# Kernel tuning notes

Hardware: AMD Instinct MI355X
Metric: run time of the kernel (lower is better)

Reference implementation:

```python
import jax, jax.numpy as jnp
import numpy as np

B, S, D = 4, 2048, 1024
H = 16
HD = D // H

def setup_inputs() -> dict:
    key = jax.random.key(0)
    ks = jax.random.split(key, 6)
    s = 0.02
    return {
        "input_tensor": jax.random.normal(ks[0], (B, S, D), dtype=jnp.float32),
        "Wq": jax.random.normal(ks[1], (D, D), dtype=jnp.float32) * s,
        "Wk": jax.random.normal(ks[2], (D, D), dtype=jnp.float32) * s,
        "Wv": jax.random.normal(ks[3], (D, D), dtype=jnp.float32) * s,
        "Wo": jax.random.normal(ks[4], (D, D), dtype=jnp.float32) * s,
        "bo": jax.random.normal(ks[5], (D,), dtype=jnp.float32) * s,
    }

def reference(input_tensor, Wq, Wk, Wv, Wo, bo):
    b, n, _ = input_tensor.shape
    # projections (nn.Linear: x @ W.T; bias=False for qkv)
    q = jnp.einsum('bnd,ed->bne', input_tensor, Wq).reshape(b, n, H, HD).transpose(0, 2, 1, 3)
    k = jnp.einsum('bnd,ed->bne', input_tensor, Wk).reshape(b, n, H, HD).transpose(0, 2, 1, 3)
    v = jnp.einsum('bnd,ed->bne', input_tensor, Wv).reshape(b, n, H, HD).transpose(0, 2, 1, 3)
    scores = jnp.einsum('bhqd,bhkd->bhqk', q, k)  # [B,H,S,S]
    causal = jnp.triu(jnp.ones((n, n), dtype=bool), k=1)
    scores = jnp.where(causal, -jnp.inf, scores)
    weights = jax.nn.softmax(scores / jnp.sqrt(jnp.float32(HD)), axis=-1)
    ctx = jnp.einsum('bhqk,bhkd->bhqd', weights, v)  # [B,H,S,HD]
    ctx = ctx.transpose(0, 2, 1, 3).reshape(b, n, D)
    return jnp.einsum('bnd,ed->bne', ctx, Wo) + bo
```

## Files before the change

kernel.cpp:

```cpp
#include <hip/hip_runtime.h>
#include <stdint.h>

#define S_LEN 2048
#define DIM   1024
#define NH    16
#define HD    64
#define BATCH 4
#define M_ROWS (BATCH * S_LEN)
#define PSTR  136

typedef __attribute__((ext_vector_type(8))) __bf16 bf16x8;
typedef __attribute__((ext_vector_type(4))) float  f32x4;

union Frag { bf16x8 v; uint4 q; };

__device__ __forceinline__ ushort f2bf(float f) {
  union { float f; unsigned u; } x; x.f = f;
  unsigned r = x.u + 0x7fffu + ((x.u >> 16) & 1u);
  return (ushort)(r >> 16);
}
__device__ __forceinline__ ushort f2bf_n(float f) {
  union { __bf16 b; ushort u; } x; x.b = (__bf16)f; return x.u;
}

__device__ __forceinline__ f32x4 mfma16(const Frag& a, const Frag& b, f32x4 c) {
  return __builtin_amdgcn_mfma_f32_16x16x32_bf16(a.v, b.v, c, 0, 0, 0);
}

__device__ __forceinline__ void gld_lds16(const ushort* g, ushort* l) {
  __builtin_amdgcn_global_load_lds(
      (__attribute__((address_space(1))) void*)g,
      (__attribute__((address_space(3))) void*)l, 16, 0, 0);
}

__global__ void cast_x_kernel(const float* __restrict__ src, ushort* __restrict__ dst) {
  int i = blockIdx.x * 256 + threadIdx.x;
  float4 f = ((const float4*)src)[i];
  ushort4 u; u.x = f2bf(f.x); u.y = f2bf(f.y); u.z = f2bf(f.z); u.w = f2bf(f.w);
  ((ushort4*)dst)[i] = u;
}

__global__ void cast_w_kernel(const float* __restrict__ w0, const float* __restrict__ w1,
                              const float* __restrict__ w2, const float* __restrict__ w3,
                              ushort* __restrict__ d0, ushort* __restrict__ d1,
                              ushort* __restrict__ d2, ushort* __restrict__ d3) {
  const float* s; ushort* d;
  int z = blockIdx.y;
  if (z == 0) { s = w0; d = d0; } else if (z == 1) { s = w1; d = d1; }
  else if (z == 2) { s = w2; d = d2; } else { s = w3; d = d3; }
  int i = blockIdx.x * 256 + threadIdx.x;
  float4 f = ((const float4*)s)[i];
  ushort4 u; u.x = f2bf(f.x); u.y = f2bf(f.y); u.z = f2bf(f.z); u.w = f2bf(f.w);
  ((ushort4*)d)[i] = u;
}

template <int MODE>
__global__ __launch_bounds__(256)
void gemm_bk64(const ushort* __restrict__ A,
               const ushort* __restrict__ B0, const ushort* __restrict__ B1,
               const ushort* __restrict__ B2,
               ushort* __restrict__ Qb, ushort* __restrict__ Kb, ushort* __restrict__ Vtb,
               float* __restrict__ outf, const float* __restrict__ bias, float scaleq) {
  __shared__ __align__(16) ushort As[128 * 64];
  __shared__ __align__(16) ushort Bs[128 * 64];
  const int K = DIM;
  int lane = threadIdx.x & 63, wave = threadIdx.x >> 6;
  int quad = lane >> 4, l15 = lane & 15;
  int rowBase = blockIdx.y * 128;
  int wsel, colBase;
  const ushort* Bt;
  if (MODE == 0) {
    wsel = blockIdx.x >> 3;
    colBase = (blockIdx.x & 7) * 128;
    Bt = (wsel == 0) ? B0 : (wsel == 1) ? B1 : B2;
  } else {
    wsel = 0;
    colBase = blockIdx.x * 128;
    Bt = B0;
  }
  int wm = (wave >> 1) * 64, wn = (wave & 1) * 64;

  const ushort* Ag = A + (size_t)rowBase * K;
  const ushort* Bg = Bt + (size_t)colBase * K;

  f32x4 acc[4][4];
#pragma unroll
  for (int i = 0; i < 4; i++)
#pragma unroll
    for (int j = 0; j < 4; j++) acc[i][j] = (f32x4){0.f, 0.f, 0.f, 0.f};

  for (int k0 = 0; k0 < K; k0 += 64) {
#pragma unroll
    for (int cc = 0; cc < 4; ++cc) {
      int c = wave * 4 + cc;
      int s = c * 64 + lane;
      int row = s >> 3;
      int c8 = (s & 7) ^ (row & 7);
      gld_lds16(Ag + (size_t)row * K + k0 + c8 * 8, &As[c * 512]);
      gld_lds16(Bg + (size_t)row * K + k0 + c8 * 8, &Bs[c * 512]);
    }
    __syncthreads();
    Frag af[4][2], bf[4][2];
#pragma unroll
    for (int t = 0; t < 4; t++) {
      int ar = wm + t * 16 + l15;
      int br = wn + t * 16 + l15;
#pragma unroll
      for (int kk = 0; kk < 2; kk++) {
        af[t][kk].q = *(const uint4*)&As[ar * 64 + (((kk * 4 + quad) ^ (ar & 7))) * 8];
        bf[t][kk].q = *(const uint4*)&Bs[br * 64 + (((kk * 4 + quad) ^ (br & 7))) * 8];
      }
    }
#pragma unroll
    for (int kk = 0; kk < 2; kk++)
#pragma unroll
      for (int i = 0; i < 4; i++)
#pragma unroll
        for (int j = 0; j < 4; j++) acc[i][j] = mfma16(af[i][kk], bf[j][kk], acc[i][j]);
    __syncthreads();
  }

#pragma unroll
  for (int i = 0; i < 4; i++) {
    int rowt = wm + i * 16 + quad * 4;
#pragma unroll
    for (int j = 0; j < 4; j++) {
      int e = colBase + wn + j * 16 + l15;
      if (MODE == 0) {
        int h = e >> 6, hd = e & 63;
        if (wsel < 2) {
          ushort* dst = wsel ? Kb : Qb;
          float sc = wsel ? 1.f : scaleq;
#pragma unroll
          for (int r = 0; r < 4; r++) {
            int m = rowBase + rowt + r;
            int b = m >> 11, s = m & (S_LEN - 1);
            dst[((size_t)((b * NH + h) * S_LEN + s) << 6) + hd] = f2bf(acc[i][j][r] * sc);
          }
        } else {
          int m0 = rowBase + rowt;
          int b = m0 >> 11, s0 = m0 & (S_LEN - 1);
          ushort4 u;
          u.x = f2bf(acc[i][j][0]); u.y = f2bf(acc[i][j][1]);
          u.z = f2bf(acc[i][j][2]); u.w = f2bf(acc[i][j][3]);
          *(ushort4*)&Vtb[((size_t)((b * NH + h) * HD + hd) << 11) + s0] = u;
        }
      } else {
        float bv = bias[e];
#pragma unroll
        for (int r = 0; r < 4; r++) {
          int m = rowBase + rowt + r;
          outf[(size_t)m * DIM + e] = acc[i][j][r] + bv;
        }
      }
    }
  }
}

__global__ __launch_bounds__(256)
void flash_attn(const ushort* __restrict__ Qb, const ushort* __restrict__ Kb,
                const ushort* __restrict__ Vtb, ushort* __restrict__ Ctx) {
  __shared__ __align__(16) ushort Ks[128 * 64];
  __shared__ __align__(16) ushort Vs[64 * 128];
  __shared__ __align__(16) ushort Ps[4][16 * PSTR];

  int lane = threadIdx.x & 63, wave = threadIdx.x >> 6;
  int quad = lane >> 4, l15 = lane & 15;
  int bh = blockIdx.x;
  int qt = (gridDim.y - 1) - blockIdx.y;
  int q0 = qt * 128, wq0 = wave * 32;

  const ushort* Qh = Qb + (size_t)bh * S_LEN * HD;
  const ushort* Kh = Kb + (size_t)bh * S_LEN * HD;
  const ushort* Vh = Vtb + (size_t)bh * HD * S_LEN;

#pragma unroll
  for (int cc = 0; cc < 4; ++cc) {
    int c = wave * 4 + cc;
    int s = c * 64 + lane;
    int row = s >> 3;
    int c8 = (s & 7) ^ (row & 7);
    gld_lds16(Qh + (size_t)(q0 + row) * HD + c8 * 8, &Ks[c * 512]);
  }
  __syncthreads();
  Frag qf[2][2];
#pragma unroll
  for (int it = 0; it < 2; ++it)
#pragma unroll
    for (int ks = 0; ks < 2; ++ks) {
      int row = wq0 + it * 16 + l15;
      int c8 = (ks * 4 + quad) ^ (row & 7);
      qf[it][ks].q = *(const uint4*)&Ks[row * 64 + c8 * 8];
    }
  __syncthreads();

  float lst[2] = {0.f, 0.f};
  f32x4 oacc[2][4];
#pragma unroll
  for (int it = 0; it < 2; ++it)
#pragma unroll
    for (int dt = 0; dt < 4; ++dt) oacc[it][dt] = (f32x4){0.f, 0.f, 0.f, 0.f};

  ushort* Pw = Ps[wave];

  for (int kt = 0; kt <= qt; ++kt) {
#pragma unroll
    for (int cc = 0; cc < 4; ++cc) {
      int c = wave * 4 + cc;
      int s = c * 64 + lane;
      int krow = s >> 3;
      int kc8 = (s & 7) ^ (krow & 7);
      gld_lds16(Kh + (size_t)(kt * 128 + krow) * HD + kc8 * 8, &Ks[c * 512]);
      int vrow = s >> 4;
      int vc8 = (s & 15) ^ (vrow & 15);
      gld_lds16(Vh + (size_t)vrow * S_LEN + kt * 128 + vc8 * 8, &Vs[c * 512]);
    }
    __syncthreads();

    f32x4 sacc[2][8];
#pragma unroll
    for (int jt = 0; jt < 8; ++jt) {
      int row = jt * 16 + l15;
      Frag kf0, kf1;
      kf0.q = *(const uint4*)&Ks[row * 64 + ((quad) ^ (row & 7)) * 8];
      kf1.q = *(const uint4*)&Ks[row * 64 + ((4 + quad) ^ (row & 7)) * 8];
#pragma unroll
      for (int it = 0; it < 2; ++it) {
        f32x4 a = (f32x4){0.f, 0.f, 0.f, 0.f};
        a = mfma16(kf0, qf[it][0], a);
        a = mfma16(kf1, qf[it][1], a);
        sacc[it][jt] = a;
      }
    }

    if (kt == qt) {
#pragma unroll
      for (int it = 0; it < 2; ++it)
#pragma unroll
        for (int jt = 0; jt < 8; ++jt)
#pragma unroll
          for (int r = 0; r < 4; ++r)
            if (jt * 16 + quad * 4 + r > wq0 + it * 16 + l15)
              sacc[it][jt][r] = -1e30f;
    }

#pragma unroll
    for (int it = 0; it < 2; ++it) {
      float ps = 0.f;
#pragma unroll
      for (int jt = 0; jt < 8; ++jt) {
        float p0 = exp2f(sacc[it][jt][0]);
        float p1 = exp2f(sacc[it][jt][1]);
        float p2 = exp2f(sacc[it][jt][2]);
        float p3 = exp2f(sacc[it][jt][3]);
        ps += (p0 + p1) + (p2 + p3);
        ushort4 u; u.x = f2bf_n(p0); u.y = f2bf_n(p1); u.z = f2bf_n(p2); u.w = f2bf_n(p3);
        *(ushort4*)&Pw[l15 * PSTR + jt * 16 + quad * 4] = u;
      }
      ps += __shfl_xor(ps, 16);
      ps += __shfl_xor(ps, 32);
      lst[it] += ps;

      Frag pf[4];
#pragma unroll
      for (int ks = 0; ks < 4; ++ks)
        pf[ks].q = *(const uint4*)&Pw[l15 * PSTR + ks * 32 + quad * 8];

#pragma unroll
      for (int dt = 0; dt < 4; ++dt) {
        f32x4 a = oacc[it][dt];
#pragma unroll
        for (int ks = 0; ks < 4; ++ks) {
          int row = dt * 16 + l15;
          Frag vf;
          vf.q = *(const uint4*)&Vs[row * 128 + (((ks * 4 + quad) ^ (row & 15))) * 8];
          a = mfma16(pf[ks], vf, a);
        }
        oacc[it][dt] = a;
      }
    }
    __syncthreads();
  }

  int b = bh >> 4, h = bh & 15;
#pragma unroll
  for (int it = 0; it < 2; ++it) {
    float linv = 1.f / lst[it];
    float lr[4];
#pragma unroll
    for (int r = 0; r < 4; ++r) lr[r] = __shfl(linv, quad * 4 + r);
#pragma unroll
    for (int r = 0; r < 4; ++r) {
      int qg = q0 + wq0 + it * 16 + quad * 4 + r;
      size_t base = ((size_t)(b * S_LEN + qg)) * DIM + h * HD;
#pragma unroll
      for (int dt = 0; dt < 4; ++dt)
        Ctx[base + dt * 16 + l15] = f2bf_n(oacc[it][dt][r] * lr[r]);
    }
  }
}

extern "C" void kernel_launch(void* const* d_in, const int* in_sizes, int n_in,
                              void* d_out, int out_size, void* d_ws, size_t ws_size,
                              hipStream_t stream) {
  (void)in_sizes; (void)n_in; (void)out_size; (void)ws_size;
  const float* x  = (const float*)d_in[0];
  const float* Wq = (const float*)d_in[1];
  const float* Wk = (const float*)d_in[2];
  const float* Wv = (const float*)d_in[3];
  const float* Wo = (const float*)d_in[4];
  const float* bo = (const float*)d_in[5];
  float* out = (float*)d_out;

  ushort* Xb  = (ushort*)d_ws;
  ushort* Wqb = Xb  + (size_t)M_ROWS * DIM;
  ushort* Wkb = Wqb + (size_t)DIM * DIM;
  ushort* Wvb = Wkb + (size_t)DIM * DIM;
  ushort* Wob = Wvb + (size_t)DIM * DIM;
  ushort* Qb  = Wob + (size_t)DIM * DIM;
  ushort* Kb  = Qb  + (size_t)M_ROWS * DIM;
  ushort* Vtb = Kb  + (size_t)M_ROWS * DIM;
  ushort* Ctx = Vtb + (size_t)M_ROWS * DIM;

  const float SCALE_Q = 0.18033688011112042f;

  cast_x_kernel<<<dim3(M_ROWS * DIM / 1024), 256, 0, stream>>>(x, Xb);
  cast_w_kernel<<<dim3(DIM * DIM / 1024, 4), 256, 0, stream>>>(Wq, Wk, Wv, Wo, Wqb, Wkb, Wvb, Wob);

  gemm_bk64<0><<<dim3(24, 64), 256, 0, stream>>>(Xb, Wqb, Wkb, Wvb, Qb, Kb, Vtb,
                                                 nullptr, nullptr, SCALE_Q);

  flash_attn<<<dim3(BATCH * NH, S_LEN / 128), 256, 0, stream>>>(Qb, Kb, Vtb, Ctx);

  gemm_bk64<1><<<dim3(8, 64), 256, 0, stream>>>(Ctx, Wob, nullptr, nullptr, nullptr, nullptr,
                                                nullptr, out, bo, 1.0f);
}
```

Before: 265.7 us.

## Reuse K smem for P, store Q/K row-major, remap GEMM blocks per XCD

The QKV GEMM now writes Q and K in plain [B*S, D] row-major layout instead of head-major, which makes those epilogue stores contiguous, and flash attention reads them with a DIM stride. The per-wave P staging buffer is removed and P is written into the K shared-memory tile after an extra barrier, with an XOR swizzle replacing the padded stride. This cuts LDS use so more blocks fit per CU, and the launch bound requests 4. GEMM block indices are also remapped so blocks dispatched to the same XCD share row tiles for L2 reuse. The cost is one more __syncthreads per KV tile in attention.

```diff
diff --git a/kernel.cpp b/kernel.cpp
--- a/kernel.cpp
+++ b/kernel.cpp
@@ -7,7 +7,6 @@
 #define HD    64
 #define BATCH 4
 #define M_ROWS (BATCH * S_LEN)
-#define PSTR  136
 
 typedef __attribute__((ext_vector_type(8))) __bf16 bf16x8;
 typedef __attribute__((ext_vector_type(4))) float  f32x4;
@@ -66,16 +65,23 @@
   const int K = DIM;
   int lane = threadIdx.x & 63, wave = threadIdx.x >> 6;
   int quad = lane >> 4, l15 = lane & 15;
-  int rowBase = blockIdx.y * 128;
+
+  const int GX = (MODE == 0) ? 24 : 8;
+  int lin = blockIdx.x + GX * blockIdx.y;
+  int xcd = lin & 7, idx = lin >> 3;
+  int by = xcd * 8 + idx / GX;
+  int bx = idx % GX;
+
+  int rowBase = by * 128;
   int wsel, colBase;
   const ushort* Bt;
   if (MODE == 0) {
-    wsel = blockIdx.x >> 3;
-    colBase = (blockIdx.x & 7) * 128;
+    wsel = bx >> 3;
+    colBase = (bx & 7) * 128;
     Bt = (wsel == 0) ? B0 : (wsel == 1) ? B1 : B2;
   } else {
     wsel = 0;
-    colBase = blockIdx.x * 128;
+    colBase = bx * 128;
     Bt = B0;
   }
   int wm = (wave >> 1) * 64, wn = (wave & 1) * 64;
@@ -127,17 +133,16 @@
     for (int j = 0; j < 4; j++) {
       int e = colBase + wn + j * 16 + l15;
       if (MODE == 0) {
-        int h = e >> 6, hd = e & 63;
         if (wsel < 2) {
           ushort* dst = wsel ? Kb : Qb;
           float sc = wsel ? 1.f : scaleq;
 #pragma unroll
           for (int r = 0; r < 4; r++) {
-            int m = rowBase + rowt + r;
-            int b = m >> 11, s = m & (S_LEN - 1);
-            dst[((size_t)((b * NH + h) * S_LEN + s) << 6) + hd] = f2bf(acc[i][j][r] * sc);
+            size_t m = (size_t)(rowBase + rowt + r);
+            dst[m * DIM + e] = f2bf(acc[i][j][r] * sc);
           }
         } else {
+          int h = e >> 6, hd = e & 63;
           int m0 = rowBase + rowt;
           int b = m0 >> 11, s0 = m0 & (S_LEN - 1);
           ushort4 u;
@@ -157,21 +162,21 @@
   }
 }
 
-__global__ __launch_bounds__(256)
+__global__ __launch_bounds__(256, 4)
 void flash_attn(const ushort* __restrict__ Qb, const ushort* __restrict__ Kb,
                 const ushort* __restrict__ Vtb, ushort* __restrict__ Ctx) {
   __shared__ __align__(16) ushort Ks[128 * 64];
   __shared__ __align__(16) ushort Vs[64 * 128];
-  __shared__ __align__(16) ushort Ps[4][16 * PSTR];
 
   int lane = threadIdx.x & 63, wave = threadIdx.x >> 6;
   int quad = lane >> 4, l15 = lane & 15;
   int bh = blockIdx.x;
   int qt = (gridDim.y - 1) - blockIdx.y;
   int q0 = qt * 128, wq0 = wave * 32;
-
-  const ushort* Qh = Qb + (size_t)bh * S_LEN * HD;
-  const ushort* Kh = Kb + (size_t)bh * S_LEN * HD;
+  int b = bh >> 4, h = bh & 15;
+
+  const ushort* Qg = Qb + (size_t)b * S_LEN * DIM + h * HD;
+  const ushort* Kg = Kb + (size_t)b * S_LEN * DIM + h * HD;
   const ushort* Vh = Vtb + (size_t)bh * HD * S_LEN;
 
 #pragma unroll
@@ -180,7 +185,7 @@
     int s = c * 64 + lane;
     int row = s >> 3;
     int c8 = (s & 7) ^ (row & 7);
-    gld_lds16(Qh + (size_t)(q0 + row) * HD + c8 * 8, &Ks[c * 512]);
+    gld_lds16(Qg + (size_t)(q0 + row) * DIM + c8 * 8, &Ks[c * 512]);
   }
   __syncthreads();
   Frag qf[2][2];
@@ -201,7 +206,7 @@
 #pragma unroll
     for (int dt = 0; dt < 4; ++dt) oacc[it][dt] = (f32x4){0.f, 0.f, 0.f, 0.f};
 
-  ushort* Pw = Ps[wave];
+  ushort* Pw = &Ks[wave * 2048];
 
   for (int kt = 0; kt <= qt; ++kt) {
 #pragma unroll
@@ -210,7 +215,7 @@
       int s = c * 64 + lane;
       int krow = s >> 3;
       int kc8 = (s & 7) ^ (krow & 7);
-      gld_lds16(Kh + (size_t)(kt * 128 + krow) * HD + kc8 * 8, &Ks[c * 512]);
+      gld_lds16(Kg + (size_t)(kt * 128 + krow) * DIM + kc8 * 8, &Ks[c * 512]);
       int vrow = s >> 4;
       int vc8 = (s & 15) ^ (vrow & 15);
       gld_lds16(Vh + (size_t)vrow * S_LEN + kt * 128 + vc8 * 8, &Vs[c * 512]);
@@ -232,6 +237,7 @@
         sacc[it][jt] = a;
       }
     }
+    __syncthreads();
 
     if (kt == qt) {
 #pragma unroll
@@ -255,7 +261,8 @@
         float p3 = exp2f(sacc[it][jt][3]);
         ps += (p0 + p1) + (p2 + p3);
         ushort4 u; u.x = f2bf_n(p0); u.y = f2bf_n(p1); u.z = f2bf_n(p2); u.w = f2bf_n(p3);
-        *(ushort4*)&Pw[l15 * PSTR + jt * 16 + quad * 4] = u;
+        int cw = (jt * 4 + quad) ^ (l15 << 1);
+        *(ushort4*)&Pw[l15 * 128 + cw * 4] = u;
       }
       ps += __shfl_xor(ps, 16);
       ps += __shfl_xor(ps, 32);
@@ -263,8 +270,10 @@
 
       Frag pf[4];
 #pragma unroll
-      for (int ks = 0; ks < 4; ++ks)
-        pf[ks].q = *(const uint4*)&Pw[l15 * PSTR + ks * 32 + quad * 8];
+      for (int ks = 0; ks < 4; ++ks) {
+        int cr = (ks * 8 + quad * 2) ^ (l15 << 1);
+        pf[ks].q = *(const uint4*)&Pw[l15 * 128 + cr * 4];
+      }
 
 #pragma unroll
       for (int dt = 0; dt < 4; ++dt) {
@@ -282,7 +291,6 @@
     __syncthreads();
   }
 
-  int b = bh >> 4, h = bh & 15;
 #pragma unroll
   for (int it = 0; it < 2; ++it) {
     float linv = 1.f / lst[it];
```

Result: slower. 442.4 us (+66.5%).
